# Optimization experiments

Hardware: AMD Instinct MI355X
Metric: run time of the kernel (lower is better)

## Reference

```python
import jax, jax.numpy as jnp
import numpy as np

DK = 128  # key/query head dim (also value dim)

def setup_inputs() -> dict:
    key = jax.random.key(0)
    k1, k2, k3, k4 = jax.random.split(key, 4)
    query = jax.random.normal(k1, (8, 512, 28, 28), dtype=jnp.float32)
    support = jax.random.normal(k2, (16, 512, 28, 28), dtype=jnp.float32)
    Wk = jax.random.normal(k3, (128, 512), dtype=jnp.float32) * (1.0 / np.sqrt(512.0))
    Wv = jax.random.normal(k4, (128, 512), dtype=jnp.float32) * (1.0 / np.sqrt(512.0))
    return {"query": query, "support": support, "Wk": Wk, "Wv": Wv}

def reference(query, support, Wk, Wv):
    B, D, H, W = query.shape
    N, Ds, Hs, Ws = support.shape
    q_flat = query.reshape(B, D, H * W)        # b d u
    s_flat = support.reshape(N, Ds, Hs * Ws)   # n d v
    # 1x1 convs == channel projections (query_head is aliased to key_head)
    q = jnp.einsum('kd,bdu->bku', Wk, q_flat)            # B dk u
    query_value = jnp.einsum('kd,bdu->bku', Wv, q_flat)  # B dv u
    support_key = jnp.einsum('kd,ndv->nkv', Wk, s_flat)  # N dk v
    support_value = jnp.einsum('kd,ndv->nkv', Wv, s_flat)  # N dv v
    scores = jnp.einsum('bku,nkv->bnuv', q, support_key) / jnp.sqrt(jnp.float32(DK))
    # first softmax over dim=3 in the source is dead code (overwritten); effective
    # attention is softmax over the support-class axis n (dim=1)
    attn = jax.nn.softmax(scores, axis=1)  # B N u v
    # note: u is summed out here, exactly as in the source einsum
    query_aligned = jnp.einsum('bnuv,nkv->bkv', attn, support_value)  # B dv v
    a = query_aligned.transpose(0, 2, 1)   # B v dv
    b = query_value.transpose(0, 2, 1)     # B u dv
    # cdist(p=2)**2 == squared euclidean distances; compute without forming diffs
    a2 = jnp.sum(a * a, axis=-1)  # B v
    b2 = jnp.sum(b * b, axis=-1)  # B u
    ab = jnp.einsum('bpd,brd->bpr', a, b)  # B v u
    d2 = jnp.maximum(a2[:, :, None] + b2[:, None, :] - 2.0 * ab, 0.0)
    P, R = d2.shape[1], d2.shape[2]
    return jnp.sum(d2, axis=(1, 2)) / (P * R)  # (B,)
```

## Files before the change

### kernel.cpp

```cpp
#include <hip/hip_runtime.h>

#define U_CNT 784
#define DKH   128
#define DD    512
#define NS    16

typedef short bf16x8 __attribute__((ext_vector_type(8)));
typedef float f32x4  __attribute__((ext_vector_type(4)));

__device__ __forceinline__ unsigned short f2bf(float f) {
  unsigned u = __builtin_bit_cast(unsigned, f);
  u += 0x7fffu + ((u >> 16) & 1u);
  return (unsigned short)(u >> 16);
}

__device__ __forceinline__ float rowg_sum(float x) {
  float a, b;
  asm("v_mov_b32 %0, %2\n\t"
      "v_mov_b32 %1, %2\n\t"
      "v_permlane16_swap_b32 %0, %1"
      : "=&v"(a), "=&v"(b) : "v"(x));
  float s = a + b;
  float c, d;
  asm("v_mov_b32 %0, %2\n\t"
      "v_mov_b32 %1, %2\n\t"
      "v_permlane32_swap_b32 %0, %1"
      : "=&v"(c), "=&v"(d) : "v"(s));
  return c + d;
}


__global__ __launch_bounds__(256)
void cast_w(const float* __restrict__ Wk, const float* __restrict__ Wv,
            unsigned short* __restrict__ Wkv_f) {
  int g = blockIdx.x * 256 + threadIdx.x;
  int fidx = g >> 6, l = g & 63;
  int f = fidx >> 4, rd = (fidx >> 2) & 3, ds = fidx & 3;
  int row = f * 16 + (l & 15);
  int dbase = rd * 128 + ds * 32 + (l >> 4) * 8;
  const float* src = (row < 128) ? (Wk + row * DD + dbase) : (Wv + (row - 128) * DD + dbase);
  unsigned short* dst = Wkv_f + (size_t)fidx * 512 + l * 8;
#pragma unroll
  for (int j = 0; j < 8; ++j) dst[j] = f2bf(src[j]);
}

__global__ __launch_bounds__(256, 4)
void proj_kernel(const float* __restrict__ query, const float* __restrict__ support,
                 const unsigned short* __restrict__ Wkv_f,
                 unsigned short* __restrict__ q_f, unsigned short* __restrict__ sk_f,
                 float* __restrict__ sv_t, float* __restrict__ S1p, float* __restrict__ S2p) {
  constexpr int PB = 16;
  constexpr int DR = 128;
  constexpr int RW = DR + 8;
  __shared__ __align__(16) unsigned short xs[2][PB * RW];
  int pc = blockIdx.x;
  int m  = blockIdx.y;
  int tid = threadIdx.x;
  int p0 = pc * PB;
  const float* X = (m < 8) ? (query + (size_t)m * DD * U_CNT)
                           : (support + (size_t)(m - 8) * DD * U_CNT);
  int r4 = tid >> 2, sub = tid & 3;
  const float* xrow = X + p0 + sub * 4;

  float4 vbuf[2];
  auto loadR = [&](int rd) {
    const float* s = xrow + (size_t)(rd * DR + r4) * U_CNT;
    vbuf[0] = *(const float4*)(s);
    vbuf[1] = *(const float4*)(s + (size_t)64 * U_CNT);
  };
  auto storeR = [&](int bb) {
    unsigned short* d0 = &xs[bb][(sub * 4) * RW + r4];
#pragma unroll
    for (int i = 0; i < 2; ++i) {
      unsigned short* dp = d0 + i * 64;
      dp[0]      = f2bf(vbuf[i].x); dp[RW]     = f2bf(vbuf[i].y);
      dp[2 * RW] = f2bf(vbuf[i].z); dp[3 * RW] = f2bf(vbuf[i].w);
    }
  };

  int wave = tid >> 6, l = tid & 63;
  int col = l & 15, rowg = l >> 4;

  f32x4 acc[4];
  f32x4 zero = {0.f, 0.f, 0.f, 0.f};
#pragma unroll
  for (int rr = 0; rr < 4; ++rr) acc[rr] = zero;

  loadR(0); storeR(0);
  __syncthreads();
  for (int rd = 0; rd < 4; ++rd) {
    if (rd < 3) loadR(rd + 1);
    int bb = rd & 1;
#pragma unroll
    for (int ds = 0; ds < 4; ++ds) {
      int dl = ds * 32 + rowg * 8;
      bf16x8 Af[4];
#pragma unroll
      for (int rr = 0; rr < 4; ++rr)
        Af[rr] = *(const bf16x8*)(Wkv_f +
                 (size_t)((((wave * 4 + rr) * 4 + rd) * 4 + ds) * 512) + l * 8);
      bf16x8 bf = *(const bf16x8*)(&xs[bb][col * RW + dl]);
#pragma unroll
      for (int rr = 0; rr < 4; ++rr)
        acc[rr] = __builtin_amdgcn_mfma_f32_16x16x32_bf16(Af[rr], bf, acc[rr], 0, 0, 0);
    }
    if (rd < 3) {
      __syncthreads();
      storeR((rd + 1) & 1);
      __syncthreads();
    }
  }

  if (m < 8) {
    if (wave < 2) {
#pragma unroll
      for (int rr = 0; rr < 4; ++rr) {
        int r = wave * 4 + rr;
        const float sc = 0.08838834764831845f * 1.4426950408889634f;
        ushort4 o;
        o.x = f2bf(acc[rr][0] * sc); o.y = f2bf(acc[rr][1] * sc);
        o.z = f2bf(acc[rr][2] * sc); o.w = f2bf(acc[rr][3] * sc);
        size_t off = (size_t)m * 100352 + (size_t)pc * 2048 +
                     (size_t)(2 * r + (rowg >> 1)) * 128 + col * 8 + (rowg & 1) * 4;
        *(ushort4*)(q_f + off) = o;
      }
    } else {
      float s1 = 0.f;
#pragma unroll
      for (int rr = 0; rr < 4; ++rr) {
        int r = wave * 4 + rr;
#pragma unroll
        for (int j = 0; j < 4; ++j) {
          float x = acc[rr][j];
          s1 += x * x;
          float xsum = x;
          xsum += __shfl_xor(xsum, 1, 64); xsum += __shfl_xor(xsum, 2, 64);
          xsum += __shfl_xor(xsum, 4, 64); xsum += __shfl_xor(xsum, 8, 64);
          if (col == 0)
            S2p[((size_t)pc * 8 + m) * DKH + (r - 8) * 16 + rowg * 4 + j] = xsum;
        }
      }
#pragma unroll
      for (int o = 32; o >= 1; o >>= 1) s1 += __shfl_xor(s1, o, 64);
      if (l == 0) S1p[((size_t)(wave - 2) * 49 + pc) * 8 + m] = s1;
    }
  } else {
    int img = m - 8;
    if (wave < 2) {
#pragma unroll
      for (int rr = 0; rr < 4; ++rr) {
        int r = wave * 4 + rr;
        ushort4 o;
        o.x = f2bf(acc[rr][0]); o.y = f2bf(acc[rr][1]);
        o.z = f2bf(acc[rr][2]); o.w = f2bf(acc[rr][3]);
        size_t off = (size_t)(p0 + col) * 2048 +
                     (size_t)(2 * r + (rowg >> 1)) * 128 + img * 8 + (rowg & 1) * 4;
        *(ushort4*)(sk_f + off) = o;
      }
    } else {
#pragma unroll
      for (int rr = 0; rr < 4; ++rr) {
        int r = wave * 4 + rr;
        int kb = (r - 8) * 16 + rowg * 4;
        float4 o = make_float4(acc[rr][0], acc[rr][1], acc[rr][2], acc[rr][3]);
        *(float4*)(sv_t + (size_t)(img * U_CNT + p0 + col) * DKH + kb) = o;
      }
    }
  }
}

__global__ __launch_bounds__(256, 3)
void score_kernel(const unsigned short* __restrict__ q_f,
                  const unsigned short* __restrict__ sk_f,
                  float* __restrict__ w_part) {
  int bx = blockIdx.x;
  int b  = bx & 7;
  int inner = bx >> 3;
  int uc = inner / 49;
  int vb = inner - uc * 49;
  int wv = threadIdx.x >> 6;
  int l  = threadIdx.x & 63;
  int col = l & 15, rowg = l >> 4;
  int vbase = vb * 16 + wv * 4;

  bf16x8 A[4][4];
#pragma unroll
  for (int v = 0; v < 4; ++v) {
    const unsigned short* ap = sk_f + (size_t)(vbase + v) * 2048 + rowg * 128 + col * 8;
#pragma unroll
    for (int s = 0; s < 4; ++s) A[v][s] = *(const bf16x8*)(ap + s * 512);
  }

  float wl[4][4];
#pragma unroll
  for (int v = 0; v < 4; ++v)
#pragma unroll
    for (int j = 0; j < 4; ++j) wl[v][j] = 0.f;

  int ut0 = (uc == 0) ? 0 : 7 + (uc - 1) * 6;
  int cnt = (uc == 0) ? 7 : 6;
  const unsigned short* qb = q_f + (size_t)b * 100352 + rowg * 128 + col * 8;
  f32x4 zero = {0.f, 0.f, 0.f, 0.f};

  const unsigned short* qp0 = qb + (size_t)ut0 * 2048;
  bf16x8 B0 = *(const bf16x8*)(qp0);
  bf16x8 B1 = *(const bf16x8*)(qp0 + 512);
  bf16x8 B2 = *(const bf16x8*)(qp0 + 1024);
  bf16x8 B3 = *(const bf16x8*)(qp0 + 1536);

  for (int it = 0; it < cnt; ++it) {
    int nit = (it + 1 < cnt) ? it + 1 : it;
    const unsigned short* qp = qb + (size_t)(ut0 + nit) * 2048;
    bf16x8 N0 = *(const bf16x8*)(qp);
    bf16x8 N1 = *(const bf16x8*)(qp + 512);
    bf16x8 N2 = *(const bf16x8*)(qp + 1024);
    bf16x8 N3 = *(const bf16x8*)(qp + 1536);

    f32x4 acc[4];
#pragma unroll
    for (int v = 0; v < 4; ++v)
      acc[v] = __builtin_amdgcn_mfma_f32_16x16x32_bf16(A[v][0], B0, zero, 0, 0, 0);
#pragma unroll
    for (int v = 0; v < 4; ++v)
      acc[v] = __builtin_amdgcn_mfma_f32_16x16x32_bf16(A[v][1], B1, acc[v], 0, 0, 0);
#pragma unroll
    for (int v = 0; v < 4; ++v)
      acc[v] = __builtin_amdgcn_mfma_f32_16x16x32_bf16(A[v][2], B2, acc[v], 0, 0, 0);
#pragma unroll
    for (int v = 0; v < 4; ++v)
      acc[v] = __builtin_amdgcn_mfma_f32_16x16x32_bf16(A[v][3], B3, acc[v], 0, 0, 0);

    float e[4][4], ps[4];
#pragma unroll
    for (int v = 0; v < 4; ++v) {
      e[v][0] = __builtin_amdgcn_exp2f(acc[v][0]);
      e[v][1] = __builtin_amdgcn_exp2f(acc[v][1]);
      e[v][2] = __builtin_amdgcn_exp2f(acc[v][2]);
      e[v][3] = __builtin_amdgcn_exp2f(acc[v][3]);
      ps[v] = (e[v][0] + e[v][1]) + (e[v][2] + e[v][3]);
    }
#pragma unroll
    for (int v = 0; v < 4; ++v) ps[v] = rowg_sum(ps[v]);
#pragma unroll
    for (int v = 0; v < 4; ++v) {
      float r = __builtin_amdgcn_rcpf(ps[v]);
      wl[v][0] += e[v][0] * r; wl[v][1] += e[v][1] * r;
      wl[v][2] += e[v][2] * r; wl[v][3] += e[v][3] * r;
    }
    B0 = N0; B1 = N1; B2 = N2; B3 = N3;
  }
#pragma unroll
  for (int v = 0; v < 4; ++v)
#pragma unroll
    for (int j = 0; j < 4; ++j) {
      float x = wl[v][j];
      x += __shfl_xor(x, 1, 64); x += __shfl_xor(x, 2, 64);
      x += __shfl_xor(x, 4, 64); x += __shfl_xor(x, 8, 64);
      wl[v][j] = x;
    }
  __shared__ float wst[4][4][16];
#pragma unroll
  for (int v = 0; v < 4; ++v)
    if (col == v) {
#pragma unroll
      for (int j = 0; j < 4; ++j) wst[wv][v][rowg * 4 + j] = wl[v][j];
    }
  __syncthreads();
  int t = threadIdx.x;
  int vl = t >> 4, c = t & 15;
  w_part[(((size_t)uc * 8 + b) * U_CNT + vb * 16 + vl) * NS + c] =
      wst[vl >> 2][vl & 3][c];
}

__global__ __launch_bounds__(256)
void align_kernel(const float* __restrict__ w_part, const float* __restrict__ sv_t,
                  float* __restrict__ T1p, float* __restrict__ T2p) {
  int vt2 = blockIdx.x;
  int t = threadIdx.x;
  __shared__ float w_sh[2][8][16];
  {
    int vl = t >> 7, b = (t >> 4) & 7, n = t & 15;
    float s = 0.f;
#pragma unroll
    for (int uc = 0; uc < 8; ++uc)
      s += w_part[(((size_t)uc * 8 + b) * U_CNT + vt2 * 2 + vl) * NS + n];
    w_sh[vl][b][n] = s;
  }
  __syncthreads();
  int k = t & 127, vl = t >> 7;
  int v = vt2 * 2 + vl;
  float a[8];
#pragma unroll
  for (int b = 0; b < 8; ++b) a[b] = 0.f;
#pragma unroll
  for (int n = 0; n < NS; ++n) {
    float s = sv_t[((size_t)n * U_CNT + v) * DKH + k];
#pragma unroll
    for (int b = 0; b < 8; ++b) a[b] += w_sh[vl][b][n] * s;
  }
  __shared__ float red[8][128];
  if (vl == 1) {
#pragma unroll
    for (int b = 0; b < 8; ++b) red[b][k] = a[b];
  }
  __syncthreads();
  if (vl == 0) {
#pragma unroll
    for (int b = 0; b < 8; ++b)
      T2p[((size_t)vt2 * 8 + b) * DKH + k] = a[b] + red[b][k];
  }
  __shared__ float sw1[4][8];
#pragma unroll
  for (int b = 0; b < 8; ++b) {
    float x = a[b] * a[b];
#pragma unroll
    for (int o = 32; o >= 1; o >>= 1) x += __shfl_xor(x, o, 64);
    if ((t & 63) == 0) sw1[t >> 6][b] = x;
  }
  __syncthreads();
  if (t < 8) T1p[vt2 * 8 + t] = sw1[0][t] + sw1[1][t] + sw1[2][t] + sw1[3][t];
}

__global__ __launch_bounds__(256)
void reduce_partials(const float* __restrict__ S1p, const float* __restrict__ T1p,
                     const float* __restrict__ S2p, const float* __restrict__ T2p,
                     float* __restrict__ S2, float* __restrict__ T2,
                     float* __restrict__ ST1) {
  __shared__ float smem[264];
  int bx = blockIdx.x, t = threadIdx.x;
  if (bx < 32) {
    int b = bx >> 2, kq = bx & 3;
    int kl = t & 31, g = t >> 5;
    int k = kq * 32 + kl;
    float s = 0.f;
    for (int w = g; w < 392; w += 8)
      s += T2p[((size_t)w * 8 + b) * DKH + k];
    smem[g * 32 + kl] = s;
    __syncthreads();
    if (t < 32) {
      float v = 0.f;
#pragma unroll
      for (int g2 = 0; g2 < 8; ++g2) v += smem[g2 * 32 + t];
      T2[b * DKH + kq * 32 + t] = v;
    }
  } else {
    int b = bx - 32;
    int k = t & 127, h = t >> 7;
    float s = 0.f;
    for (int w = h; w < 49; w += 2)
      s += S2p[((size_t)w * 8 + b) * DKH + k];
    if (h == 1) smem[k] = s;
    __syncthreads();
    if (h == 0) S2[b * DKH + k] = s + smem[k];
    float c = 0.f;
    for (int i = t; i < 98; i += 256)  c += S1p[i * 8 + b];
    for (int i = t; i < 392; i += 256) c += T1p[i * 8 + b];
#pragma unroll
    for (int o = 32; o >= 1; o >>= 1) c += __shfl_xor(c, o, 64);
    if ((t & 63) == 0) smem[256 + (t >> 6)] = c;
    __syncthreads();
    if (t == 0) ST1[b] = smem[256] + smem[257] + smem[258] + smem[259];
  }
}

__global__ void final_kernel(const float* __restrict__ S2, const float* __restrict__ T2,
                             const float* __restrict__ ST1, float* __restrict__ out) {
  int b = blockIdx.x, t = threadIdx.x;
  float p = S2[b * DKH + t] * T2[b * DKH + t];
#pragma unroll
  for (int o = 32; o >= 1; o >>= 1) p += __shfl_xor(p, o, 64);
  __shared__ float s2[2];
  if ((t & 63) == 0) s2[t >> 6] = p;
  __syncthreads();
  if (t == 0)
    out[b] = (784.0f * ST1[b] - 2.0f * (s2[0] + s2[1])) * (1.0f / (784.0f * 784.0f));
}

extern "C" void kernel_launch(void* const* d_in, const int* in_sizes, int n_in,
                              void* d_out, int out_size, void* d_ws, size_t ws_size,
                              hipStream_t stream) {
  const float* query   = (const float*)d_in[0];
  const float* support = (const float*)d_in[1];
  const float* Wk      = (const float*)d_in[2];
  const float* Wv      = (const float*)d_in[3];
  float* out = (float*)d_out;
  char* ws = (char*)d_ws;

  unsigned short* Wkv  = (unsigned short*)(ws + 0);
  unsigned short* q_f  = (unsigned short*)(ws + 262144);
  unsigned short* sk_f = (unsigned short*)(ws + 1867776);
  float*          sv_t = (float*)(ws + 5079040);
  float*          w_part = (float*)(ws + 11501568);
  float*          S1p  = (float*)(ws + 14712832);
  float*          T1p  = (float*)(ws + 14716928);
  float*          S2p  = (float*)(ws + 14733312);
  float*          T2p  = (float*)(ws + 14934016);
  float*          S2   = (float*)(ws + 16539648);
  float*          T2   = (float*)(ws + 16543744);
  float*          ST1  = (float*)(ws + 16547840);
  if (ws_size < (size_t)16548000) return;

  cast_w<<<64, 256, 0, stream>>>(Wk, Wv, Wkv);
  proj_kernel<<<dim3(49, 24), 256, 0, stream>>>(query, support, Wkv, q_f, sk_f, sv_t, S1p, S2p);
  score_kernel<<<3136, 256, 0, stream>>>(q_f, sk_f, w_part);
  align_kernel<<<392, 256, 0, stream>>>(w_part, sv_t, T1p, T2p);
  reduce_partials<<<40, 256, 0, stream>>>(S1p, T1p, S2p, T2p, S2, T2, ST1);
  final_kernel<<<8, 128, 0, stream>>>(S2, T2, ST1, out);
}
```

Measured before the change: 151.8 us.

## Fuse align stage into score kernel and drop u-chunk split

The score kernel now loops over all 49 u-tiles itself instead of splitting u into 8 chunks. Each wave handles 2 v positions instead of 4, and the grid shrinks from 3136 to 784 blocks. With full weights available in-block, it applies the support-value weighting directly and writes T1/T2 partials, which removes the w_part buffer and the separate align kernel launch. The trade-off is fewer blocks each doing a longer serial loop, so parallelism and latency hiding drop, and sv_t is re-read once per batch.

```diff
diff --git a/kernel.cpp b/kernel.cpp
--- a/kernel.cpp
+++ b/kernel.cpp
@@ -172,67 +172,63 @@
 __global__ __launch_bounds__(256, 3)
 void score_kernel(const unsigned short* __restrict__ q_f,
                   const unsigned short* __restrict__ sk_f,
-                  float* __restrict__ w_part) {
+                  const float* __restrict__ sv_t,
+                  float* __restrict__ T1p, float* __restrict__ T2p) {
   int bx = blockIdx.x;
   int b  = bx & 7;
-  int inner = bx >> 3;
-  int uc = inner / 49;
-  int vb = inner - uc * 49;
+  int vb = bx >> 3;
   int wv = threadIdx.x >> 6;
   int l  = threadIdx.x & 63;
   int col = l & 15, rowg = l >> 4;
-  int vbase = vb * 16 + wv * 4;
-
-  bf16x8 A[4][4];
-#pragma unroll
-  for (int v = 0; v < 4; ++v) {
+  int vbase = vb * 8 + wv * 2;
+
+  bf16x8 A[2][4];
+#pragma unroll
+  for (int v = 0; v < 2; ++v) {
     const unsigned short* ap = sk_f + (size_t)(vbase + v) * 2048 + rowg * 128 + col * 8;
 #pragma unroll
     for (int s = 0; s < 4; ++s) A[v][s] = *(const bf16x8*)(ap + s * 512);
   }
 
-  float wl[4][4];
-#pragma unroll
-  for (int v = 0; v < 4; ++v)
+  float wl[2][4];
+#pragma unroll
+  for (int v = 0; v < 2; ++v)
 #pragma unroll
     for (int j = 0; j < 4; ++j) wl[v][j] = 0.f;
 
-  int ut0 = (uc == 0) ? 0 : 7 + (uc - 1) * 6;
-  int cnt = (uc == 0) ? 7 : 6;
   const unsigned short* qb = q_f + (size_t)b * 100352 + rowg * 128 + col * 8;
   f32x4 zero = {0.f, 0.f, 0.f, 0.f};
 
-  const unsigned short* qp0 = qb + (size_t)ut0 * 2048;
-  bf16x8 B0 = *(const bf16x8*)(qp0);
-  bf16x8 B1 = *(const bf16x8*)(qp0 + 512);
-  bf16x8 B2 = *(const bf16x8*)(qp0 + 1024);
-  bf16x8 B3 = *(const bf16x8*)(qp0 + 1536);
-
-  for (int it = 0; it < cnt; ++it) {
-    int nit = (it + 1 < cnt) ? it + 1 : it;
-    const unsigned short* qp = qb + (size_t)(ut0 + nit) * 2048;
+  bf16x8 B0 = *(const bf16x8*)(qb);
+  bf16x8 B1 = *(const bf16x8*)(qb + 512);
+  bf16x8 B2 = *(const bf16x8*)(qb + 1024);
+  bf16x8 B3 = *(const bf16x8*)(qb + 1536);
+
+  for (int it = 0; it < 49; ++it) {
+    int nit = (it + 1 < 49) ? it + 1 : it;
+    const unsigned short* qp = qb + (size_t)nit * 2048;
     bf16x8 N0 = *(const bf16x8*)(qp);
     bf16x8 N1 = *(const bf16x8*)(qp + 512);
     bf16x8 N2 = *(const bf16x8*)(qp + 1024);
     bf16x8 N3 = *(const bf16x8*)(qp + 1536);
 
-    f32x4 acc[4];
-#pragma unroll
-    for (int v = 0; v < 4; ++v)
+    f32x4 acc[2];
+#pragma unroll
+    for (int v = 0; v < 2; ++v)
       acc[v] = __builtin_amdgcn_mfma_f32_16x16x32_bf16(A[v][0], B0, zero, 0, 0, 0);
 #pragma unroll
-    for (int v = 0; v < 4; ++v)
+    for (int v = 0; v < 2; ++v)
       acc[v] = __builtin_amdgcn_mfma_f32_16x16x32_bf16(A[v][1], B1, acc[v], 0, 0, 0);
 #pragma unroll
-    for (int v = 0; v < 4; ++v)
+    for (int v = 0; v < 2; ++v)
       acc[v] = __builtin_amdgcn_mfma_f32_16x16x32_bf16(A[v][2], B2, acc[v], 0, 0, 0);
 #pragma unroll
-    for (int v = 0; v < 4; ++v)
+    for (int v = 0; v < 2; ++v)
       acc[v] = __builtin_amdgcn_mfma_f32_16x16x32_bf16(A[v][3], B3, acc[v], 0, 0, 0);
 
-    float e[4][4], ps[4];
-#pragma unroll
-    for (int v = 0; v < 4; ++v) {
+    float e[2][4], ps[2];
+#pragma unroll
+    for (int v = 0; v < 2; ++v) {
       e[v][0] = __builtin_amdgcn_exp2f(acc[v][0]);
       e[v][1] = __builtin_amdgcn_exp2f(acc[v][1]);
       e[v][2] = __builtin_amdgcn_exp2f(acc[v][2]);
@@ -240,17 +236,18 @@
       ps[v] = (e[v][0] + e[v][1]) + (e[v][2] + e[v][3]);
     }
 #pragma unroll
-    for (int v = 0; v < 4; ++v) ps[v] = rowg_sum(ps[v]);
-#pragma unroll
-    for (int v = 0; v < 4; ++v) {
+    for (int v = 0; v < 2; ++v) ps[v] = rowg_sum(ps[v]);
+#pragma unroll
+    for (int v = 0; v < 2; ++v) {
       float r = __builtin_amdgcn_rcpf(ps[v]);
       wl[v][0] += e[v][0] * r; wl[v][1] += e[v][1] * r;
       wl[v][2] += e[v][2] * r; wl[v][3] += e[v][3] * r;
     }
     B0 = N0; B1 = N1; B2 = N2; B3 = N3;
   }
-#pragma unroll
-  for (int v = 0; v < 4; ++v)
+
+#pragma unroll
+  for (int v = 0; v < 2; ++v)
 #pragma unroll
     for (int j = 0; j < 4; ++j) {
       float x = wl[v][j];
@@ -258,67 +255,40 @@
       x += __shfl_xor(x, 4, 64); x += __shfl_xor(x, 8, 64);
       wl[v][j] = x;
     }
-  __shared__ float wst[4][4][16];
-#pragma unroll
-  for (int v = 0; v < 4; ++v)
+  __shared__ float wst[4][2][16];
+#pragma unroll
+  for (int v = 0; v < 2; ++v)
     if (col == v) {
 #pragma unroll
       for (int j = 0; j < 4; ++j) wst[wv][v][rowg * 4 + j] = wl[v][j];
     }
+  __syncthreads();
+
+  __shared__ float red[4][128];
+  __shared__ float t1s[4];
+  int k0 = l * 2;
+  float a00 = 0.f, a01 = 0.f, a10 = 0.f, a11 = 0.f;
+#pragma unroll
+  for (int n = 0; n < NS; ++n) {
+    float w0 = wst[wv][0][n], w1 = wst[wv][1][n];
+    const float* p0 = sv_t + ((size_t)n * U_CNT + vbase) * DKH + k0;
+    float2 s0 = *(const float2*)(p0);
+    float2 s1 = *(const float2*)(p0 + DKH);
+    a00 += w0 * s0.x; a01 += w0 * s0.y;
+    a10 += w1 * s1.x; a11 += w1 * s1.y;
+  }
+  float t1 = a00 * a00 + a01 * a01 + a10 * a10 + a11 * a11;
+  red[wv][k0] = a00 + a10;
+  red[wv][k0 + 1] = a01 + a11;
+#pragma unroll
+  for (int o = 32; o >= 1; o >>= 1) t1 += __shfl_xor(t1, o, 64);
+  if (l == 0) t1s[wv] = t1;
   __syncthreads();
   int t = threadIdx.x;
-  int vl = t >> 4, c = t & 15;
-  w_part[(((size_t)uc * 8 + b) * U_CNT + vb * 16 + vl) * NS + c] =
-      wst[vl >> 2][vl & 3][c];
-}
-
-__global__ __launch_bounds__(256)
-void align_kernel(const float* __restrict__ w_part, const float* __restrict__ sv_t,
-                  float* __restrict__ T1p, float* __restrict__ T2p) {
-  int vt2 = blockIdx.x;
-  int t = threadIdx.x;
-  __shared__ float w_sh[2][8][16];
-  {
-    int vl = t >> 7, b = (t >> 4) & 7, n = t & 15;
-    float s = 0.f;
-#pragma unroll
-    for (int uc = 0; uc < 8; ++uc)
-      s += w_part[(((size_t)uc * 8 + b) * U_CNT + vt2 * 2 + vl) * NS + n];
-    w_sh[vl][b][n] = s;
-  }
-  __syncthreads();
-  int k = t & 127, vl = t >> 7;
-  int v = vt2 * 2 + vl;
-  float a[8];
-#pragma unroll
-  for (int b = 0; b < 8; ++b) a[b] = 0.f;
-#pragma unroll
-  for (int n = 0; n < NS; ++n) {
-    float s = sv_t[((size_t)n * U_CNT + v) * DKH + k];
-#pragma unroll
-    for (int b = 0; b < 8; ++b) a[b] += w_sh[vl][b][n] * s;
-  }
-  __shared__ float red[8][128];
-  if (vl == 1) {
-#pragma unroll
-    for (int b = 0; b < 8; ++b) red[b][k] = a[b];
-  }
-  __syncthreads();
-  if (vl == 0) {
-#pragma unroll
-    for (int b = 0; b < 8; ++b)
-      T2p[((size_t)vt2 * 8 + b) * DKH + k] = a[b] + red[b][k];
-  }
-  __shared__ float sw1[4][8];
-#pragma unroll
-  for (int b = 0; b < 8; ++b) {
-    float x = a[b] * a[b];
-#pragma unroll
-    for (int o = 32; o >= 1; o >>= 1) x += __shfl_xor(x, o, 64);
-    if ((t & 63) == 0) sw1[t >> 6][b] = x;
-  }
-  __syncthreads();
-  if (t < 8) T1p[vt2 * 8 + t] = sw1[0][t] + sw1[1][t] + sw1[2][t] + sw1[3][t];
+  if (t < 128)
+    T2p[((size_t)vb * 8 + b) * DKH + t] = red[0][t] + red[1][t] + red[2][t] + red[3][t];
+  if (t == 128)
+    T1p[vb * 8 + b] = t1s[0] + t1s[1] + t1s[2] + t1s[3];
 }
 
 __global__ __launch_bounds__(256)
@@ -333,7 +303,7 @@
     int kl = t & 31, g = t >> 5;
     int k = kq * 32 + kl;
     float s = 0.f;
-    for (int w = g; w < 392; w += 8)
+    for (int w = g; w < 98; w += 8)
       s += T2p[((size_t)w * 8 + b) * DKH + k];
     smem[g * 32 + kl] = s;
     __syncthreads();
@@ -353,8 +323,8 @@
     __syncthreads();
     if (h == 0) S2[b * DKH + k] = s + smem[k];
     float c = 0.f;
-    for (int i = t; i < 98; i += 256)  c += S1p[i * 8 + b];
-    for (int i = t; i < 392; i += 256) c += T1p[i * 8 + b];
+    for (int i = t; i < 98; i += 256) c += S1p[i * 8 + b];
+    for (int i = t; i < 98; i += 256) c += T1p[i * 8 + b];
 #pragma unroll
     for (int o = 32; o >= 1; o >>= 1) c += __shfl_xor(c, o, 64);
     if ((t & 63) == 0) smem[256 + (t >> 6)] = c;
@@ -390,20 +360,18 @@
   unsigned short* q_f  = (unsigned short*)(ws + 262144);
   unsigned short* sk_f = (unsigned short*)(ws + 1867776);
   float*          sv_t = (float*)(ws + 5079040);
-  float*          w_part = (float*)(ws + 11501568);
-  float*          S1p  = (float*)(ws + 14712832);
-  float*          T1p  = (float*)(ws + 14716928);
-  float*          S2p  = (float*)(ws + 14733312);
-  float*          T2p  = (float*)(ws + 14934016);
-  float*          S2   = (float*)(ws + 16539648);
-  float*          T2   = (float*)(ws + 16543744);
-  float*          ST1  = (float*)(ws + 16547840);
-  if (ws_size < (size_t)16548000) return;
+  float*          T1p  = (float*)(ws + 11501568);
+  float*          S1p  = (float*)(ws + 11504896);
+  float*          S2p  = (float*)(ws + 11508224);
+  float*          T2p  = (float*)(ws + 11708928);
+  float*          S2   = (float*)(ws + 12110336);
+  float*          T2   = (float*)(ws + 12114432);
+  float*          ST1  = (float*)(ws + 12118528);
+  if (ws_size < (size_t)12118784) return;
 
   cast_w<<<64, 256, 0, stream>>>(Wk, Wv, Wkv);
   proj_kernel<<<dim3(49, 24), 256, 0, stream>>>(query, support, Wkv, q_f, sk_f, sv_t, S1p, S2p);
-  score_kernel<<<3136, 256, 0, stream>>>(q_f, sk_f, w_part);
-  align_kernel<<<392, 256, 0, stream>>>(w_part, sv_t, T1p, T2p);
+  score_kernel<<<784, 256, 0, stream>>>(q_f, sk_f, sv_t, T1p, T2p);
   reduce_partials<<<40, 256, 0, stream>>>(S1p, T1p, S2p, T2p, S2, T2, ST1);
   final_kernel<<<8, 128, 0, stream>>>(S2, T2, ST1, out);
 }
```

Result: no change. 149.2 us (-1.7%).
